# Kernel optimization log

Hardware: AMD Instinct MI355X
Metric: run time of the kernel (lower is better)

## Reference

```python
import jax, jax.numpy as jnp
import numpy as np

SEQ = 256  # position axis length fixed by the graph's iota(256)


def _mod(freq, phase):
    # sin(2*pi*t*freq + phase)^2 * 0.1 + 1 - 0.05, shape [SEQ]
    t = jnp.arange(SEQ, dtype=jnp.float32)
    return jnp.sin(t * (2.0 * jnp.pi) * freq + phase) ** 2 * 0.1 + 0.95


def setup_inputs() -> dict:
    key = jax.random.key(0)
    ks = jax.random.split(key, 16)
    K = 2048  # number of scattered index triples
    return {
        "primals_1": jax.random.normal(ks[0], (6, 256, 256), jnp.float32),
        "primals_2": jax.random.normal(ks[1], (12, 6, 256), jnp.float32),
        "primals_3": jax.random.normal(ks[2], (6, 256, 256), jnp.float32),
        "primals_4": jax.random.normal(ks[3], (6, 256), jnp.float32),
        "primals_5": jax.random.randint(ks[4], (K,), 0, 6),
        "primals_6": jax.random.randint(ks[5], (K,), 0, 256),
        "primals_7": jax.random.randint(ks[6], (K,), 0, 256),
        "primals_8": jax.random.randint(ks[7], (K,), 0, 256),
        "primals_9": jax.random.uniform(ks[8], (1,), jnp.float32),
        "primals_10": jax.random.uniform(ks[9], (1,), jnp.float32),
        "primals_11": jax.random.normal(ks[10], (6, 256), jnp.float32),
        "primals_12": jax.random.uniform(ks[11], (1,), jnp.float32),
        "primals_13": jax.random.uniform(ks[12], (1,), jnp.float32),
        "primals_14": jax.random.normal(ks[13], (6, 256), jnp.float32),
        "primals_15": jax.random.uniform(ks[14], (1,), jnp.float32),
        "primals_16": jax.random.uniform(ks[15], (1,), jnp.float32),
    }


def reference(primals_1, primals_2, primals_3, primals_4, primals_5, primals_6,
              primals_7, primals_8, primals_9, primals_10, primals_11, primals_12,
              primals_13, primals_14, primals_15, primals_16):
    decay = primals_3 * 0.975  # reused in all three stages

    def stage(q, table, freq, phase):
        # gather from table [6,256] at (p5,p6) -> [K]
        vals = table[primals_5, primals_6]
        # scatter into a fresh copy of the persistent buffer, then decay-accumulate
        mem = primals_1.at[primals_5, primals_7, primals_8].set(vals) + decay  # [6,256,256]
        # bmm 'attention': q [12,6,256] x mem [6,256,256] -> [12,6,256]
        att = jnp.einsum('hbd,bde->hbe', q, mem)
        return att, _mod(freq, phase)

    a1, m1 = stage(primals_2, primals_4, primals_9, primals_10)
    x1 = a1 / m1
    a2, m2 = stage(x1, primals_11, primals_12, primals_13)
    x2 = a2 * m2
    a3, m3 = stage(x2, primals_14, primals_15, primals_16)
    return a3 / m3
```

## Files before the change

### kernel.cpp

```cpp
#include <hip/hip_runtime.h>
#include <hip/hip_fp16.h>

#define TWO_PI 6.2831853071795864769f


__global__ __launch_bounds__(1024) void prep_kernel(
    const float* __restrict__ P1, const float* __restrict__ P3,
    const int* __restrict__ p5, const int* __restrict__ p6,
    const int* __restrict__ p7, const int* __restrict__ p8,
    const float* __restrict__ T4, const float* __restrict__ T11,
    const float* __restrict__ T14,
    __half* __restrict__ Ch, int* __restrict__ cnt,
    int* __restrict__ wde_g, float* __restrict__ wv_g, int K)
{
    const int tid = (int)threadIdx.x;
    const int blk = (int)blockIdx.x;
    if (blk < 96) {
        int i = blk * 1024 + tid;
        float4 a = ((const float4*)P1)[i];
        float4 c = ((const float4*)P3)[i];
        __half2 h0 = __floats2half2_rn(fmaf(c.x, 0.975f, a.x),
                                       fmaf(c.y, 0.975f, a.y));
        __half2 h1 = __floats2half2_rn(fmaf(c.z, 0.975f, a.z),
                                       fmaf(c.w, 0.975f, a.w));
        __half2* dst = (__half2*)Ch + (i << 1);
        dst[0] = h0;
        dst[1] = h1;
        return;
    }

    __shared__ unsigned pk[2048];
    __shared__ unsigned hmap[4096];
    __shared__ int scnt[8];
    for (int k = tid; k < K; k += 1024)
        pk[k] = ((unsigned)p5[k] << 24) | ((unsigned)p6[k] << 16) |
                ((unsigned)p7[k] << 8) | (unsigned)p8[k];
    for (int i = tid; i < 4096; i += 1024) hmap[i] = 0xFFFFFFFFu;
    if (tid < 8) scnt[tid] = 0;
    __syncthreads();

    for (int k = tid; k < K; k += 1024) {
        unsigned v = pk[k];
        unsigned key  = v & 0xFFFFu;
        unsigned full = (key << 3) | (v >> 24);
        unsigned mine = (full << 12) | (unsigned)k;
        unsigned hh = (full * 2654435761u) >> 20;
        for (;;) {
            unsigned prev = atomicCAS(&hmap[hh], 0xFFFFFFFFu, mine);
            if (prev == 0xFFFFFFFFu) break;
            if ((prev >> 12) == full) { atomicMax(&hmap[hh], mine); break; }
            hh = (hh + 1) & 4095u;
        }
    }
    __syncthreads();

    for (int k = tid; k < K; k += 1024) {
        unsigned v = pk[k];
        unsigned key  = v & 0xFFFFu;
        unsigned full = (key << 3) | (v >> 24);
        unsigned hh = (full * 2654435761u) >> 20;
        unsigned cur;
        for (;;) {
            cur = hmap[hh];
            if ((cur >> 12) == full) break;
            hh = (hh + 1) & 4095u;
        }
        if ((cur & 0xFFFu) == (unsigned)k) {
            int b = (int)(v >> 24), c = (int)((v >> 16) & 0xFFu);
            float p1v = P1[(b << 16) | key];
            int w = atomicAdd(&scnt[b], 1);
            wde_g[b * 2048 + w] = (int)key;
            wv_g[(0 * 6 + b) * 2048 + w] = T4 [b * 256 + c] - p1v;
            wv_g[(1 * 6 + b) * 2048 + w] = T11[b * 256 + c] - p1v;
            wv_g[(2 * 6 + b) * 2048 + w] = T14[b * 256 + c] - p1v;
        }
    }
    __syncthreads();
    if (tid < 8) cnt[tid] = scnt[tid];
}

__global__ __launch_bounds__(1024, 4) void chain_kernel(
    const __half* __restrict__ Ch, const float* __restrict__ P2,
    const int* __restrict__ cnt, const int* __restrict__ wde_g,
    const float* __restrict__ wv_g,
    const float* __restrict__ f1, const float* __restrict__ ph1,
    const float* __restrict__ f2, const float* __restrict__ ph2,
    const float* __restrict__ f3, const float* __restrict__ ph3,
    float* __restrict__ out)
{
    const int blk = (int)blockIdx.x;
    const int b = blk & 7;
    if (b >= 6) return;
    const int h = blk >> 3;

    __shared__ float v[256];
    __shared__ float pv[16][256];
    __shared__ float modl[3][256];
    __shared__ unsigned short wde[2048];
    __shared__ float wv0[2048], wv1[2048], wv2[2048];

    const int tid = (int)threadIdx.x;
    const int dg = tid >> 6;
    const int eg = tid & 63;

    const __half2* Chv = (const __half2*)Ch +
                         ((((b << 8) + (dg << 4)) << 7) + (eg << 1));
    float4 m4[16];
    #pragma unroll
    for (int i = 0; i < 16; ++i) {
        __half2 lo = Chv[(i << 7)];
        __half2 hi = Chv[(i << 7) + 1];
        float2 f0 = __half22float2(lo);
        float2 f1v = __half22float2(hi);
        m4[i] = make_float4(f0.x, f0.y, f1v.x, f1v.y);
    }

    if (tid < 256) v[tid] = P2[(h * 6 + b) * 256 + tid];
    if (tid < 768) {
        int s = tid >> 8, ee = tid & 255;
        float fr = (s == 0) ? f1[0]  : (s == 1) ? f2[0]  : f3[0];
        float ph = (s == 0) ? ph1[0] : (s == 1) ? ph2[0] : ph3[0];
        float sn = __sinf((float)ee * TWO_PI * fr + ph);
        float mm = sn * sn * 0.1f + 0.95f;
        modl[s][ee] = (s == 1) ? mm : 1.0f / mm;
    }
    const int nwl = cnt[b];
    for (int i = tid; i < nwl; i += 1024) {
        wde[i] = (unsigned short)wde_g[b * 2048 + i];
        wv0[i] = wv_g[(0 * 6 + b) * 2048 + i];
        wv1[i] = wv_g[(1 * 6 + b) * 2048 + i];
        wv2[i] = wv_g[(2 * 6 + b) * 2048 + i];
    }
    __syncthreads();

    const int e256 = tid & 255;
    for (int s = 0; s < 3; ++s) {
        float4 acc = make_float4(0.f, 0.f, 0.f, 0.f);
        #pragma unroll
        for (int j = 0; j < 4; ++j) {
            float4 vv = *(const float4*)&v[(dg << 4) + (j << 2)];
            float4 m0 = m4[(j << 2) + 0];
            float4 m1 = m4[(j << 2) + 1];
            float4 m2 = m4[(j << 2) + 2];
            float4 m3 = m4[(j << 2) + 3];
            acc.x = fmaf(vv.x, m0.x, acc.x); acc.y = fmaf(vv.x, m0.y, acc.y);
            acc.z = fmaf(vv.x, m0.z, acc.z); acc.w = fmaf(vv.x, m0.w, acc.w);
            acc.x = fmaf(vv.y, m1.x, acc.x); acc.y = fmaf(vv.y, m1.y, acc.y);
            acc.z = fmaf(vv.y, m1.z, acc.z); acc.w = fmaf(vv.y, m1.w, acc.w);
            acc.x = fmaf(vv.z, m2.x, acc.x); acc.y = fmaf(vv.z, m2.y, acc.y);
            acc.z = fmaf(vv.z, m2.z, acc.z); acc.w = fmaf(vv.z, m2.w, acc.w);
            acc.x = fmaf(vv.w, m3.x, acc.x); acc.y = fmaf(vv.w, m3.y, acc.y);
            acc.z = fmaf(vv.w, m3.z, acc.z); acc.w = fmaf(vv.w, m3.w, acc.w);
        }
        *(float4*)&pv[dg][eg << 2] = acc;
        __syncthreads();
        {
            int r = tid >> 8;
            float x = pv[r][e256] + pv[r + 4][e256] +
                      pv[r + 8][e256] + pv[r + 12][e256];
            __syncthreads();
            pv[r][e256] = x;
        }
        __syncthreads();
        if (tid < 256)
            pv[0][tid] = (pv[0][tid] + pv[1][tid]) + (pv[2][tid] + pv[3][tid]);
        __syncthreads();
        const float* wvs = (s == 0) ? wv0 : (s == 1) ? wv1 : wv2;
        for (int i = tid; i < nwl; i += 1024) {
            unsigned de = wde[i];
            atomicAdd(&pv[0][de & 255u], v[de >> 8] * wvs[i]);
        }
        __syncthreads();
        if (tid < 256)
            v[tid] = pv[0][tid] * modl[s][tid];
        __syncthreads();
    }
    if (tid < 256) out[(h * 6 + b) * 256 + tid] = v[tid];
}

extern "C" void kernel_launch(void* const* d_in, const int* in_sizes, int n_in,
                              void* d_out, int out_size, void* d_ws, size_t ws_size,
                              hipStream_t stream)
{
    (void)n_in; (void)out_size; (void)ws_size;
    const float* P1  = (const float*)d_in[0];
    const float* P2  = (const float*)d_in[1];
    const float* P3  = (const float*)d_in[2];
    const float* T4  = (const float*)d_in[3];
    const int*   p5  = (const int*)d_in[4];
    const int*   p6  = (const int*)d_in[5];
    const int*   p7  = (const int*)d_in[6];
    const int*   p8  = (const int*)d_in[7];
    const float* f1  = (const float*)d_in[8];
    const float* ph1 = (const float*)d_in[9];
    const float* T11 = (const float*)d_in[10];
    const float* f2  = (const float*)d_in[11];
    const float* ph2 = (const float*)d_in[12];
    const float* T14 = (const float*)d_in[13];
    const float* f3  = (const float*)d_in[14];
    const float* ph3 = (const float*)d_in[15];
    float* out = (float*)d_out;
    int K = in_sizes[4];

    char* ws = (char*)d_ws;
    __half* Ch   = (__half*)(ws);
    int*   cnt   = (int*)  (ws + 786432);
    int*   wde_g = (int*)  (ws + 786496);
    float* wv_g  = (float*)(ws + 835648);

    hipLaunchKernelGGL(prep_kernel, dim3(97), dim3(1024), 0, stream,
                       P1, P3, p5, p6, p7, p8, T4, T11, T14,
                       Ch, cnt, wde_g, wv_g, K);
    hipLaunchKernelGGL(chain_kernel, dim3(96), dim3(1024), 0, stream,
                       Ch, P2, cnt, wde_g, wv_g,
                       f1, ph1, f2, ph2, f3, ph3, out);
}
```

Before: 23.98 us.

## Fuse prep and chain kernels into one launch with flag-based inter-block sync

Merges the prep kernel and the chain kernel into a single launch. Producer blocks signal completion through global atomic flags, and consumer blocks spin-wait on those flags before loading the fp16 matrix and the dedup lists. Consumer blocks also compute their setup (v, modulation tables) before waiting, so that setup overlaps the producers. This removes one kernel launch boundary but adds a memset and relies on all 169 blocks being co-resident to avoid deadlock. It also relies on relaxed atomics, with no acquire/release fences, being enough for visibility.

```diff
diff --git a/kernel.cpp b/kernel.cpp
--- a/kernel.cpp
+++ b/kernel.cpp
@@ -4,116 +4,116 @@
 #define TWO_PI 6.2831853071795864769f
 
 
-__global__ __launch_bounds__(1024) void prep_kernel(
-    const float* __restrict__ P1, const float* __restrict__ P3,
+__global__ __launch_bounds__(1024, 4) void mega_kernel(
+    const float* __restrict__ P1, const float* __restrict__ P2,
+    const float* __restrict__ P3, const float* __restrict__ T4,
     const int* __restrict__ p5, const int* __restrict__ p6,
     const int* __restrict__ p7, const int* __restrict__ p8,
-    const float* __restrict__ T4, const float* __restrict__ T11,
-    const float* __restrict__ T14,
+    const float* __restrict__ f1, const float* __restrict__ ph1,
+    const float* __restrict__ T11, const float* __restrict__ f2,
+    const float* __restrict__ ph2, const float* __restrict__ T14,
+    const float* __restrict__ f3, const float* __restrict__ ph3,
     __half* __restrict__ Ch, int* __restrict__ cnt,
-    int* __restrict__ wde_g, float* __restrict__ wv_g, int K)
+    int* __restrict__ wde_g, float* __restrict__ wv_g,
+    int* __restrict__ flags, float* __restrict__ out, int K)
 {
+    __shared__ __align__(16) unsigned char smem[49216];
     const int tid = (int)threadIdx.x;
     const int blk = (int)blockIdx.x;
+
     if (blk < 96) {
         int i = blk * 1024 + tid;
         float4 a = ((const float4*)P1)[i];
         float4 c = ((const float4*)P3)[i];
-        __half2 h0 = __floats2half2_rn(fmaf(c.x, 0.975f, a.x),
-                                       fmaf(c.y, 0.975f, a.y));
-        __half2 h1 = __floats2half2_rn(fmaf(c.z, 0.975f, a.z),
-                                       fmaf(c.w, 0.975f, a.w));
-        __half2* dst = (__half2*)Ch + (i << 1);
-        dst[0] = h0;
-        dst[1] = h1;
+        union { __half2 h2[2]; unsigned long long u; } pk_;
+        pk_.h2[0] = __floats2half2_rn(fmaf(c.x, 0.975f, a.x),
+                                      fmaf(c.y, 0.975f, a.y));
+        pk_.h2[1] = __floats2half2_rn(fmaf(c.z, 0.975f, a.z),
+                                      fmaf(c.w, 0.975f, a.w));
+        __hip_atomic_store((unsigned long long*)Ch + i, pk_.u,
+                           __ATOMIC_RELAXED, __HIP_MEMORY_SCOPE_AGENT);
+        __syncthreads();
+        if (tid == 0)
+            __hip_atomic_fetch_add(&flags[0], 1, __ATOMIC_RELAXED,
+                                   __HIP_MEMORY_SCOPE_AGENT);
         return;
     }
 
-    __shared__ unsigned pk[2048];
-    __shared__ unsigned hmap[4096];
-    __shared__ int scnt[8];
-    for (int k = tid; k < K; k += 1024)
-        pk[k] = ((unsigned)p5[k] << 24) | ((unsigned)p6[k] << 16) |
-                ((unsigned)p7[k] << 8) | (unsigned)p8[k];
-    for (int i = tid; i < 4096; i += 1024) hmap[i] = 0xFFFFFFFFu;
-    if (tid < 8) scnt[tid] = 0;
-    __syncthreads();
-
-    for (int k = tid; k < K; k += 1024) {
-        unsigned v = pk[k];
-        unsigned key  = v & 0xFFFFu;
-        unsigned full = (key << 3) | (v >> 24);
-        unsigned mine = (full << 12) | (unsigned)k;
-        unsigned hh = (full * 2654435761u) >> 20;
-        for (;;) {
-            unsigned prev = atomicCAS(&hmap[hh], 0xFFFFFFFFu, mine);
-            if (prev == 0xFFFFFFFFu) break;
-            if ((prev >> 12) == full) { atomicMax(&hmap[hh], mine); break; }
-            hh = (hh + 1) & 4095u;
-        }
-    }
-    __syncthreads();
-
-    for (int k = tid; k < K; k += 1024) {
-        unsigned v = pk[k];
-        unsigned key  = v & 0xFFFFu;
-        unsigned full = (key << 3) | (v >> 24);
-        unsigned hh = (full * 2654435761u) >> 20;
-        unsigned cur;
-        for (;;) {
-            cur = hmap[hh];
-            if ((cur >> 12) == full) break;
-            hh = (hh + 1) & 4095u;
-        }
-        if ((cur & 0xFFFu) == (unsigned)k) {
-            int b = (int)(v >> 24), c = (int)((v >> 16) & 0xFFu);
-            float p1v = P1[(b << 16) | key];
-            int w = atomicAdd(&scnt[b], 1);
-            wde_g[b * 2048 + w] = (int)key;
-            wv_g[(0 * 6 + b) * 2048 + w] = T4 [b * 256 + c] - p1v;
-            wv_g[(1 * 6 + b) * 2048 + w] = T11[b * 256 + c] - p1v;
-            wv_g[(2 * 6 + b) * 2048 + w] = T14[b * 256 + c] - p1v;
-        }
-    }
-    __syncthreads();
-    if (tid < 8) cnt[tid] = scnt[tid];
-}
-
-__global__ __launch_bounds__(1024, 4) void chain_kernel(
-    const __half* __restrict__ Ch, const float* __restrict__ P2,
-    const int* __restrict__ cnt, const int* __restrict__ wde_g,
-    const float* __restrict__ wv_g,
-    const float* __restrict__ f1, const float* __restrict__ ph1,
-    const float* __restrict__ f2, const float* __restrict__ ph2,
-    const float* __restrict__ f3, const float* __restrict__ ph3,
-    float* __restrict__ out)
-{
-    const int blk = (int)blockIdx.x;
-    const int b = blk & 7;
-    if (b >= 6) return;
-    const int h = blk >> 3;
-
-    __shared__ float v[256];
-    __shared__ float pv[16][256];
-    __shared__ float modl[3][256];
-    __shared__ unsigned short wde[2048];
-    __shared__ float wv0[2048], wv1[2048], wv2[2048];
-
-    const int tid = (int)threadIdx.x;
-    const int dg = tid >> 6;
-    const int eg = tid & 63;
-
-    const __half2* Chv = (const __half2*)Ch +
-                         ((((b << 8) + (dg << 4)) << 7) + (eg << 1));
-    float4 m4[16];
-    #pragma unroll
-    for (int i = 0; i < 16; ++i) {
-        __half2 lo = Chv[(i << 7)];
-        __half2 hi = Chv[(i << 7) + 1];
-        float2 f0 = __half22float2(lo);
-        float2 f1v = __half22float2(hi);
-        m4[i] = make_float4(f0.x, f0.y, f1v.x, f1v.y);
-    }
+    if (blk == 168) {
+        unsigned* pk   = (unsigned*)smem;
+        unsigned* hmap = (unsigned*)(smem + 8192);
+        int*      scnt = (int*)(smem + 24576);
+        for (int k = tid; k < K; k += 1024)
+            pk[k] = ((unsigned)p5[k] << 24) | ((unsigned)p6[k] << 16) |
+                    ((unsigned)p7[k] << 8) | (unsigned)p8[k];
+        for (int i = tid; i < 4096; i += 1024) hmap[i] = 0xFFFFFFFFu;
+        if (tid < 8) scnt[tid] = 0;
+        __syncthreads();
+        for (int k = tid; k < K; k += 1024) {
+            unsigned v = pk[k];
+            unsigned key  = v & 0xFFFFu;
+            unsigned full = (key << 3) | (v >> 24);
+            unsigned mine = (full << 12) | (unsigned)k;
+            unsigned hh = (full * 2654435761u) >> 20;
+            for (;;) {
+                unsigned prev = atomicCAS(&hmap[hh], 0xFFFFFFFFu, mine);
+                if (prev == 0xFFFFFFFFu) break;
+                if ((prev >> 12) == full) { atomicMax(&hmap[hh], mine); break; }
+                hh = (hh + 1) & 4095u;
+            }
+        }
+        __syncthreads();
+        for (int k = tid; k < K; k += 1024) {
+            unsigned v = pk[k];
+            unsigned key  = v & 0xFFFFu;
+            unsigned full = (key << 3) | (v >> 24);
+            unsigned hh = (full * 2654435761u) >> 20;
+            unsigned cur;
+            for (;;) {
+                cur = hmap[hh];
+                if ((cur >> 12) == full) break;
+                hh = (hh + 1) & 4095u;
+            }
+            if ((cur & 0xFFFu) == (unsigned)k) {
+                int b = (int)(v >> 24), c = (int)((v >> 16) & 0xFFu);
+                float p1v = P1[(b << 16) | key];
+                int w = atomicAdd(&scnt[b], 1);
+                __hip_atomic_store(&wde_g[b * 2048 + w], (int)key,
+                                   __ATOMIC_RELAXED, __HIP_MEMORY_SCOPE_AGENT);
+                __hip_atomic_store(&wv_g[(0 * 6 + b) * 2048 + w],
+                                   T4[b * 256 + c] - p1v,
+                                   __ATOMIC_RELAXED, __HIP_MEMORY_SCOPE_AGENT);
+                __hip_atomic_store(&wv_g[(1 * 6 + b) * 2048 + w],
+                                   T11[b * 256 + c] - p1v,
+                                   __ATOMIC_RELAXED, __HIP_MEMORY_SCOPE_AGENT);
+                __hip_atomic_store(&wv_g[(2 * 6 + b) * 2048 + w],
+                                   T14[b * 256 + c] - p1v,
+                                   __ATOMIC_RELAXED, __HIP_MEMORY_SCOPE_AGENT);
+            }
+        }
+        __syncthreads();
+        if (tid < 8)
+            __hip_atomic_store(&cnt[tid], scnt[tid],
+                               __ATOMIC_RELAXED, __HIP_MEMORY_SCOPE_AGENT);
+        __syncthreads();
+        if (tid == 0)
+            __hip_atomic_store(&flags[1], 1,
+                               __ATOMIC_RELAXED, __HIP_MEMORY_SCOPE_AGENT);
+        return;
+    }
+
+    const int cid = blk - 96;
+    const int h = cid / 6, b = cid - (cid / 6) * 6;
+    const int dg = tid >> 6, eg = tid & 63;
+
+    float* v             = (float*)smem;
+    float (*pv)[256]     = (float(*)[256])(smem + 1024);
+    float (*modl)[256]   = (float(*)[256])(smem + 17408);
+    unsigned short* wde  = (unsigned short*)(smem + 20480);
+    float* wv0           = (float*)(smem + 24576);
+    float* wv1           = (float*)(smem + 32768);
+    float* wv2           = (float*)(smem + 40960);
+    int*   nw_s          = (int*)(smem + 49152);
 
     if (tid < 256) v[tid] = P2[(h * 6 + b) * 256 + tid];
     if (tid < 768) {
@@ -124,12 +124,41 @@
         float mm = sn * sn * 0.1f + 0.95f;
         modl[s][ee] = (s == 1) ? mm : 1.0f / mm;
     }
-    const int nwl = cnt[b];
+    __syncthreads();
+
+    if (tid == 0) {
+        while (__hip_atomic_load(&flags[0], __ATOMIC_RELAXED,
+                                 __HIP_MEMORY_SCOPE_AGENT) < 96)
+            __builtin_amdgcn_s_sleep(1);
+    }
+    __syncthreads();
+
+    const unsigned long long* Cq =
+        (const unsigned long long*)Ch + (((b << 8) + (dg << 4)) << 6) + eg;
+    unsigned long long mraw[16];
+    #pragma unroll
+    for (int i = 0; i < 16; ++i)
+        mraw[i] = __hip_atomic_load(Cq + (i << 6), __ATOMIC_RELAXED,
+                                    __HIP_MEMORY_SCOPE_AGENT);
+
+    if (tid == 0) {
+        while (__hip_atomic_load(&flags[1], __ATOMIC_RELAXED,
+                                 __HIP_MEMORY_SCOPE_AGENT) == 0)
+            __builtin_amdgcn_s_sleep(1);
+        *nw_s = __hip_atomic_load(&cnt[b], __ATOMIC_RELAXED,
+                                  __HIP_MEMORY_SCOPE_AGENT);
+    }
+    __syncthreads();
+    const int nwl = *nw_s;
     for (int i = tid; i < nwl; i += 1024) {
-        wde[i] = (unsigned short)wde_g[b * 2048 + i];
-        wv0[i] = wv_g[(0 * 6 + b) * 2048 + i];
-        wv1[i] = wv_g[(1 * 6 + b) * 2048 + i];
-        wv2[i] = wv_g[(2 * 6 + b) * 2048 + i];
+        wde[i] = (unsigned short)__hip_atomic_load(
+            &wde_g[b * 2048 + i], __ATOMIC_RELAXED, __HIP_MEMORY_SCOPE_AGENT);
+        wv0[i] = __hip_atomic_load(&wv_g[(0 * 6 + b) * 2048 + i],
+                                   __ATOMIC_RELAXED, __HIP_MEMORY_SCOPE_AGENT);
+        wv1[i] = __hip_atomic_load(&wv_g[(1 * 6 + b) * 2048 + i],
+                                   __ATOMIC_RELAXED, __HIP_MEMORY_SCOPE_AGENT);
+        wv2[i] = __hip_atomic_load(&wv_g[(2 * 6 + b) * 2048 + i],
+                                   __ATOMIC_RELAXED, __HIP_MEMORY_SCOPE_AGENT);
     }
     __syncthreads();
 
@@ -139,18 +168,19 @@
         #pragma unroll
         for (int j = 0; j < 4; ++j) {
             float4 vv = *(const float4*)&v[(dg << 4) + (j << 2)];
-            float4 m0 = m4[(j << 2) + 0];
-            float4 m1 = m4[(j << 2) + 1];
-            float4 m2 = m4[(j << 2) + 2];
-            float4 m3 = m4[(j << 2) + 3];
-            acc.x = fmaf(vv.x, m0.x, acc.x); acc.y = fmaf(vv.x, m0.y, acc.y);
-            acc.z = fmaf(vv.x, m0.z, acc.z); acc.w = fmaf(vv.x, m0.w, acc.w);
-            acc.x = fmaf(vv.y, m1.x, acc.x); acc.y = fmaf(vv.y, m1.y, acc.y);
-            acc.z = fmaf(vv.y, m1.z, acc.z); acc.w = fmaf(vv.y, m1.w, acc.w);
-            acc.x = fmaf(vv.z, m2.x, acc.x); acc.y = fmaf(vv.z, m2.y, acc.y);
-            acc.z = fmaf(vv.z, m2.z, acc.z); acc.w = fmaf(vv.z, m2.w, acc.w);
-            acc.x = fmaf(vv.w, m3.x, acc.x); acc.y = fmaf(vv.w, m3.y, acc.y);
-            acc.z = fmaf(vv.w, m3.z, acc.z); acc.w = fmaf(vv.w, m3.w, acc.w);
+            #pragma unroll
+            for (int i = 0; i < 4; ++i) {
+                union { unsigned long long u; __half2 h2[2]; } cv;
+                cv.u = mraw[(j << 2) + i];
+                float2 f01 = __half22float2(cv.h2[0]);
+                float2 f23 = __half22float2(cv.h2[1]);
+                float vd = (i == 0) ? vv.x : (i == 1) ? vv.y
+                         : (i == 2) ? vv.z : vv.w;
+                acc.x = fmaf(vd, f01.x, acc.x);
+                acc.y = fmaf(vd, f01.y, acc.y);
+                acc.z = fmaf(vd, f23.x, acc.z);
+                acc.w = fmaf(vd, f23.y, acc.w);
+            }
         }
         *(float4*)&pv[dg][eg << 2] = acc;
         __syncthreads();
@@ -207,11 +237,11 @@
     int*   cnt   = (int*)  (ws + 786432);
     int*   wde_g = (int*)  (ws + 786496);
     float* wv_g  = (float*)(ws + 835648);
-
-    hipLaunchKernelGGL(prep_kernel, dim3(97), dim3(1024), 0, stream,
-                       P1, P3, p5, p6, p7, p8, T4, T11, T14,
-                       Ch, cnt, wde_g, wv_g, K);
-    hipLaunchKernelGGL(chain_kernel, dim3(96), dim3(1024), 0, stream,
-                       Ch, P2, cnt, wde_g, wv_g,
-                       f1, ph1, f2, ph2, f3, ph3, out);
+    int*   flags = (int*)  (ws + 983104);
+
+    hipMemsetAsync(flags, 0, 64, stream);
+    hipLaunchKernelGGL(mega_kernel, dim3(169), dim3(1024), 0, stream,
+                       P1, P2, P3, T4, p5, p6, p7, p8,
+                       f1, ph1, T11, f2, ph2, T14, f3, ph3,
+                       Ch, cnt, wde_g, wv_g, flags, out, K);
 }
```

Result: slower. 31.38 us (+30.9%).

## Repartition matvec into 32 row groups with packed fp16 registers and single-pass reduction

Applied to the files above, without the earlier changes.

Each thread now owns 8 rows by 8 columns of the fp16 matrix tile instead of 16 rows by 4 columns. It keeps the raw fp16 data packed in registers as 128-bit loads and converts to float inside the loop rather than holding 64 floats. The partial sums grow to 32 row groups and are reduced by 256 threads in one pass, which removes two barriers per stage. In exchange, shared memory for partials doubles and the final reduction is serial over 32 entries per thread with fewer threads active.

```diff
diff --git a/kernel.cpp b/kernel.cpp
--- a/kernel.cpp
+++ b/kernel.cpp
@@ -94,26 +94,19 @@
     const int h = blk >> 3;
 
     __shared__ float v[256];
-    __shared__ float pv[16][256];
+    __shared__ float pv[32][256];
     __shared__ float modl[3][256];
     __shared__ unsigned short wde[2048];
     __shared__ float wv0[2048], wv1[2048], wv2[2048];
 
     const int tid = (int)threadIdx.x;
-    const int dg = tid >> 6;
-    const int eg = tid & 63;
-
-    const __half2* Chv = (const __half2*)Ch +
-                         ((((b << 8) + (dg << 4)) << 7) + (eg << 1));
-    float4 m4[16];
+    const int dg = tid >> 5;
+    const int eg = tid & 31;
+
+    const ulonglong2* Cq = (const ulonglong2*)Ch + (b << 13) + (dg << 8) + eg;
+    ulonglong2 mraw[8];
     #pragma unroll
-    for (int i = 0; i < 16; ++i) {
-        __half2 lo = Chv[(i << 7)];
-        __half2 hi = Chv[(i << 7) + 1];
-        float2 f0 = __half22float2(lo);
-        float2 f1v = __half22float2(hi);
-        m4[i] = make_float4(f0.x, f0.y, f1v.x, f1v.y);
-    }
+    for (int i = 0; i < 8; ++i) mraw[i] = Cq[i << 5];
 
     if (tid < 256) v[tid] = P2[(h * 6 + b) * 256 + tid];
     if (tid < 768) {
@@ -133,37 +126,36 @@
     }
     __syncthreads();
 
-    const int e256 = tid & 255;
     for (int s = 0; s < 3; ++s) {
-        float4 acc = make_float4(0.f, 0.f, 0.f, 0.f);
+        float4 alo = make_float4(0.f, 0.f, 0.f, 0.f);
+        float4 ahi = make_float4(0.f, 0.f, 0.f, 0.f);
         #pragma unroll
-        for (int j = 0; j < 4; ++j) {
-            float4 vv = *(const float4*)&v[(dg << 4) + (j << 2)];
-            float4 m0 = m4[(j << 2) + 0];
-            float4 m1 = m4[(j << 2) + 1];
-            float4 m2 = m4[(j << 2) + 2];
-            float4 m3 = m4[(j << 2) + 3];
-            acc.x = fmaf(vv.x, m0.x, acc.x); acc.y = fmaf(vv.x, m0.y, acc.y);
-            acc.z = fmaf(vv.x, m0.z, acc.z); acc.w = fmaf(vv.x, m0.w, acc.w);
-            acc.x = fmaf(vv.y, m1.x, acc.x); acc.y = fmaf(vv.y, m1.y, acc.y);
-            acc.z = fmaf(vv.y, m1.z, acc.z); acc.w = fmaf(vv.y, m1.w, acc.w);
-            acc.x = fmaf(vv.z, m2.x, acc.x); acc.y = fmaf(vv.z, m2.y, acc.y);
-            acc.z = fmaf(vv.z, m2.z, acc.z); acc.w = fmaf(vv.z, m2.w, acc.w);
-            acc.x = fmaf(vv.w, m3.x, acc.x); acc.y = fmaf(vv.w, m3.y, acc.y);
-            acc.z = fmaf(vv.w, m3.z, acc.z); acc.w = fmaf(vv.w, m3.w, acc.w);
-        }
-        *(float4*)&pv[dg][eg << 2] = acc;
-        __syncthreads();
-        {
-            int r = tid >> 8;
-            float x = pv[r][e256] + pv[r + 4][e256] +
-                      pv[r + 8][e256] + pv[r + 12][e256];
-            __syncthreads();
-            pv[r][e256] = x;
-        }
-        __syncthreads();
-        if (tid < 256)
-            pv[0][tid] = (pv[0][tid] + pv[1][tid]) + (pv[2][tid] + pv[3][tid]);
+        for (int i = 0; i < 8; ++i) {
+            float vv = v[(dg << 3) + i];
+            union { unsigned long long u; __half2 h2[2]; } lo, hi;
+            lo.u = mraw[i].x;
+            hi.u = mraw[i].y;
+            float2 c0 = __half22float2(lo.h2[0]);
+            float2 c1 = __half22float2(lo.h2[1]);
+            float2 c2 = __half22float2(hi.h2[0]);
+            float2 c3 = __half22float2(hi.h2[1]);
+            alo.x = fmaf(vv, c0.x, alo.x); alo.y = fmaf(vv, c0.y, alo.y);
+            alo.z = fmaf(vv, c1.x, alo.z); alo.w = fmaf(vv, c1.y, alo.w);
+            ahi.x = fmaf(vv, c2.x, ahi.x); ahi.y = fmaf(vv, c2.y, ahi.y);
+            ahi.z = fmaf(vv, c3.x, ahi.z); ahi.w = fmaf(vv, c3.y, ahi.w);
+        }
+        *(float4*)&pv[dg][(eg << 3)]     = alo;
+        *(float4*)&pv[dg][(eg << 3) + 4] = ahi;
+        __syncthreads();
+        if (tid < 256) {
+            float x0 = 0.f, x1 = 0.f, x2 = 0.f, x3 = 0.f;
+            #pragma unroll
+            for (int g = 0; g < 32; g += 4) {
+                x0 += pv[g][tid];     x1 += pv[g + 1][tid];
+                x2 += pv[g + 2][tid]; x3 += pv[g + 3][tid];
+            }
+            pv[0][tid] = (x0 + x1) + (x2 + x3);
+        }
         __syncthreads();
         const float* wvs = (s == 0) ? wv0 : (s == 1) ? wv1 : wv2;
         for (int i = tid; i < nwl; i += 1024) {
```

New measurement: 23.54 us. Within noise of the previous version (-1.8%).
